# Kernel tuning notes

Measured on AMD Instinct MI355X. Metric: run time of the kernel, lower is better.

The kernel has to match this reference:

```python
import jax, jax.numpy as jnp
import numpy as np

B = 1 << 20
EMB = 8
N_BREEDS, N_TEMPS = 15, 9
HIDDENS = [128, 64, 32]
IN_DIM = (EMB * 2 + 9) * 2  # 50
EPS = 1e-5


def _encode_pet(breed, size, energy, temp, age, social, weight, breed_emb, temp_emb):
    # breed/temp: [B] int -> embedding gather [B,8]; size/energy -> one-hot [B,3]
    be = breed_emb[breed]
    te = temp_emb[temp]
    size_oh = jax.nn.one_hot(size, 3, dtype=be.dtype)
    energy_oh = jax.nn.one_hot(energy, 3, dtype=be.dtype)
    nums = jnp.stack([age / 15.0, social, weight / 100.0], axis=-1)  # [B,3]
    return jnp.concatenate([be, size_oh, energy_oh, te, nums], axis=-1)  # [B,25]


def _mlp(x, Ws, bs, gammas, betas, Wout, bout):
    for W, b, g, bt in zip(Ws, bs, gammas, betas):
        x = x @ W + b
        mu = jnp.mean(x, axis=0)
        var = jnp.mean(jnp.square(x - mu), axis=0)  # biased var (torch BN training)
        x = (x - mu) * jax.lax.rsqrt(var + EPS) * g + bt
        x = jax.nn.relu(x)
    x = x @ Wout + bout
    return jax.nn.sigmoid(x).squeeze(-1)  # [B]


def setup_inputs() -> dict:
    key = jax.random.key(0)
    ks = jax.random.split(key, 32)
    inp = {
        "pet1_breed": jax.random.randint(ks[0], (B,), 0, N_BREEDS, dtype=jnp.int32),
        "pet1_size": jax.random.randint(ks[1], (B,), 0, 3, dtype=jnp.int32),
        "pet1_energy": jax.random.randint(ks[2], (B,), 0, 3, dtype=jnp.int32),
        "pet1_temp": jax.random.randint(ks[3], (B,), 0, N_TEMPS, dtype=jnp.int32),
        "pet1_age": jax.random.uniform(ks[4], (B,)) * 15.0,
        "pet1_social": jax.random.uniform(ks[5], (B,)),
        "pet1_weight": jax.random.uniform(ks[6], (B,)) * 100.0,
        "pet2_breed": jax.random.randint(ks[7], (B,), 0, N_BREEDS, dtype=jnp.int32),
        "pet2_size": jax.random.randint(ks[8], (B,), 0, 3, dtype=jnp.int32),
        "pet2_energy": jax.random.randint(ks[9], (B,), 0, 3, dtype=jnp.int32),
        "pet2_temp": jax.random.randint(ks[10], (B,), 0, N_TEMPS, dtype=jnp.int32),
        "pet2_age": jax.random.uniform(ks[11], (B,)) * 15.0,
        "pet2_social": jax.random.uniform(ks[12], (B,)),
        "pet2_weight": jax.random.uniform(ks[13], (B,)) * 100.0,
        "breed_emb": jax.random.normal(ks[14], (N_BREEDS, EMB), dtype=jnp.float32),
        "temp_emb": jax.random.normal(ks[15], (N_TEMPS, EMB), dtype=jnp.float32),
    }
    prev = IN_DIM
    ki = 16
    for i, h in enumerate(HIDDENS, start=1):
        s = 1.0 / np.sqrt(prev)
        inp[f"W{i}"] = jax.random.uniform(ks[ki], (prev, h), minval=-s, maxval=s); ki += 1
        inp[f"b{i}"] = jax.random.uniform(ks[ki], (h,), minval=-s, maxval=s); ki += 1
        inp[f"gamma{i}"] = jnp.ones((h,), jnp.float32)
        inp[f"beta{i}"] = jnp.zeros((h,), jnp.float32)
        prev = h
    s = 1.0 / np.sqrt(prev)
    inp["W4"] = jax.random.uniform(ks[ki], (prev, 1), minval=-s, maxval=s); ki += 1
    inp["b4"] = jax.random.uniform(ks[ki], (1,), minval=-s, maxval=s)
    return inp


def reference(pet1_breed, pet1_size, pet1_energy, pet1_temp, pet1_age, pet1_social, pet1_weight,
              pet2_breed, pet2_size, pet2_energy, pet2_temp, pet2_age, pet2_social, pet2_weight,
              breed_emb, temp_emb,
              W1, b1, gamma1, beta1, W2, b2, gamma2, beta2, W3, b3, gamma3, beta3, W4, b4):
    f1 = _encode_pet(pet1_breed, pet1_size, pet1_energy, pet1_temp,
                     pet1_age, pet1_social, pet1_weight, breed_emb, temp_emb)
    f2 = _encode_pet(pet2_breed, pet2_size, pet2_energy, pet2_temp,
                     pet2_age, pet2_social, pet2_weight, breed_emb, temp_emb)
    x = jnp.concatenate([f1, f2], axis=-1)  # [B,50]
    return _mlp(x, [W1, W2, W3], [b1, b2, b3], [gamma1, gamma2, gamma3],
                [beta1, beta2, beta3], W4, b4)
```

## Files before the change

kernel.cpp:

```cpp
#include <hip/hip_runtime.h>
#include <hip/hip_bf16.h>

#define BATCH (1u<<20)
static constexpr float EPSBN = 1e-5f;
static constexpr float INV_B = 1.0f / (float)BATCH;

typedef unsigned int   uint;
typedef unsigned short ushort;
typedef unsigned long long u64;

#define TSTR 132
#define NTABROWS 66
#define OFF_W2F    55296ULL
#define OFF_W3F    71680ULL
#define OFF_STATS  75776ULL
#define OFF_PARAMS 90112ULL
#define OFF_W1S    94208ULL
#define OFF_X2     147456ULL
#define OFF_X1     (147456ULL + 134217728ULL)
#define OFF_X3T3   (OFF_X1 + 268435456ULL)
#define T1_NEED    (147456ULL + 134217728ULL)
#define T2_NEED    (OFF_X1 + 67108864ULL)
#define T3_NEED    (OFF_X3T3 + 67108864ULL)

struct Ptrs {
  const int *br1,*sz1,*en1,*tp1; const float *ag1,*so1,*wt1;
  const int *br2,*sz2,*en2,*tp2; const float *ag2,*so2,*wt2;
  const float *bemb,*temb;
  const float *W1,*b1,*g1,*be1;
  const float *W2,*b2,*g2,*be2;
  const float *W3,*b3,*g3,*be3;
  const float *W4,*b4;
  float* ws; float* out;
};

typedef __attribute__((ext_vector_type(8))) short bf16x8;
typedef __attribute__((ext_vector_type(4))) float f32x4;

__device__ __forceinline__ float4 ld4(const float* p) {
  return *reinterpret_cast<const float4*>(p);
}
__device__ __forceinline__ float4 f4add(float4 a, float4 b) {
  return make_float4(a.x+b.x, a.y+b.y, a.z+b.z, a.w+b.w);
}
__device__ __forceinline__ float4 f4fma(float4 a, float4 w, float s) {
  return make_float4(fmaf(w.x,s,a.x), fmaf(w.y,s,a.y), fmaf(w.z,s,a.z), fmaf(w.w,s,a.w));
}
__device__ __forceinline__ void add4(float4& a, const float4 b) {
  a.x += b.x; a.y += b.y; a.z += b.z; a.w += b.w;
}
__device__ __forceinline__ void fma4s(float4& a, const float4 b, float s) {
  a.x = fmaf(b.x, s, a.x); a.y = fmaf(b.y, s, a.y);
  a.z = fmaf(b.z, s, a.z); a.w = fmaf(b.w, s, a.w);
}

__device__ __forceinline__ ushort bfb(float f) {
  union { __hip_bfloat16 h; ushort u; } cv; cv.h = __float2bfloat16(f); return cv.u;
}
__device__ __forceinline__ uint pk2(float a, float b) {
  return ((uint)bfb(b) << 16) | (uint)bfb(a);
}
__device__ __forceinline__ uint pku(ushort a, ushort b) {
  return ((uint)b << 16) | (uint)a;
}
__device__ __forceinline__ bf16x8 ldfrag(const void* p) {
  union { uint4 u; bf16x8 v; } cv; cv.u = *reinterpret_cast<const uint4*>(p); return cv.v;
}
__device__ __forceinline__ bf16x8 mkfrag(uint a, uint b, uint c, uint d) {
  union { uint4 u; bf16x8 v; } cv; cv.u = make_uint4(a,b,c,d); return cv.v;
}
__device__ __forceinline__ float bflo(uint w) { return __uint_as_float(w << 16); }
__device__ __forceinline__ float bfhi(uint w) { return __uint_as_float(w & 0xffff0000u); }
__device__ __forceinline__ float bf2f(ushort u) { return __uint_as_float(((uint)u) << 16); }

struct SIdx { int r[8]; float v[6]; };
__device__ __forceinline__ SIdx load_idx(const Ptrs& P, unsigned s) {
  SIdx o;
  o.r[0] = P.br1[s];      o.r[1] = 15 + P.tp1[s];
  o.r[2] = 24 + P.br2[s]; o.r[3] = 39 + P.tp2[s];
  o.r[4] = 48 + P.sz1[s]; o.r[5] = 51 + P.en1[s];
  o.r[6] = 54 + P.sz2[s]; o.r[7] = 57 + P.en2[s];
  o.v[0] = P.ag1[s]*(1.0f/15.0f); o.v[1] = P.so1[s]; o.v[2] = P.wt1[s]*0.01f;
  o.v[3] = P.ag2[s]*(1.0f/15.0f); o.v[4] = P.so2[s]; o.v[5] = P.wt2[s]*0.01f;
  return o;
}

__device__ __forceinline__ float4 gather4(const float* Tl, const float* contT,
                                          const int rb[8], const float v[6], int c) {
  float4 A = f4add(f4add(ld4(Tl+rb[0]+c), ld4(Tl+rb[1]+c)),
                   f4add(ld4(Tl+rb[2]+c), ld4(Tl+rb[3]+c)));
  float4 B = f4add(f4add(ld4(Tl+rb[4]+c), ld4(Tl+rb[5]+c)),
                   f4add(ld4(Tl+rb[6]+c), ld4(Tl+rb[7]+c)));
  A = f4fma(A, ld4(contT + 60*TSTR + c), v[0]);
  A = f4fma(A, ld4(contT + 61*TSTR + c), v[1]);
  A = f4fma(A, ld4(contT + 62*TSTR + c), v[2]);
  B = f4fma(B, ld4(contT + 63*TSTR + c), v[3]);
  B = f4fma(B, ld4(contT + 64*TSTR + c), v[4]);
  B = f4fma(B, ld4(contT + 65*TSTR + c), v[5]);
  return f4add(A, B);
}

__device__ __forceinline__ void load_rb(const Ptrs& P, unsigned s, int rb[8], float v[6]) {
  SIdx o = load_idx(P, s);
  #pragma unroll
  for (int i = 0; i < 8; ++i) rb[i] = o.r[i]*TSTR;
  #pragma unroll
  for (int i = 0; i < 6; ++i) v[i] = o.v[i];
}

__device__ __forceinline__ void stage_tab(const float* wsT, const float* params,
                                          float* Tl, bool bn1) {
  for (int i = threadIdx.x; i < NTABROWS*TSTR; i += blockDim.x) Tl[i] = wsT[i];
  if (bn1) {
    for (int i = threadIdx.x; i < 128; i += blockDim.x) {
      Tl[66*TSTR + i] = params[i];
      Tl[67*TSTR + i] = params[128 + i];
    }
  }
  __syncthreads();
}

__device__ __forceinline__ void x2_from_lds(const float* Tl, const int rb[8], const float v[6],
                                            const float* W2, const float* b2, float4 acc[16]) {
  #pragma unroll
  for (int j4 = 0; j4 < 16; ++j4) acc[j4] = ld4(b2 + j4*4);
  #pragma unroll 1
  for (int c4 = 0; c4 < 32; ++c4) {
    const int c = c4 * 4;
    float4 x = gather4(Tl, Tl, rb, v, c);
    const float4 sc = *reinterpret_cast<const float4*>(Tl + 66*TSTR + c);
    const float4 sh = *reinterpret_cast<const float4*>(Tl + 67*TSTR + c);
    float hv[4];
    hv[0] = fmaxf(fmaf(x.x, sc.x, sh.x), 0.0f);
    hv[1] = fmaxf(fmaf(x.y, sc.y, sh.y), 0.0f);
    hv[2] = fmaxf(fmaf(x.z, sc.z, sh.z), 0.0f);
    hv[3] = fmaxf(fmaf(x.w, sc.w, sh.w), 0.0f);
    #pragma unroll
    for (int r = 0; r < 4; ++r) {
      const float hr = hv[r];
      const float4* w = reinterpret_cast<const float4*>(W2 + (c + r)*64);
      #pragma unroll
      for (int j4 = 0; j4 < 16; ++j4) fma4s(acc[j4], w[j4], hr);
    }
  }
}

__device__ __forceinline__ void x3_from_acc2(const float4 acc2[16], const Ptrs& P,
                                             const float* sc2, const float* sh2,
                                             float4 acc3[8]) {
  #pragma unroll
  for (int j4 = 0; j4 < 8; ++j4) acc3[j4] = ld4(P.b3 + j4*4);
  #pragma unroll
  for (int k4 = 0; k4 < 16; ++k4) {
    const float4 a = acc2[k4];
    const float4 sc = ld4(sc2 + k4*4), sh = ld4(sh2 + k4*4);
    const float hr[4] = {
      fmaxf(fmaf(a.x, sc.x, sh.x), 0.0f),
      fmaxf(fmaf(a.y, sc.y, sh.y), 0.0f),
      fmaxf(fmaf(a.z, sc.z, sh.z), 0.0f),
      fmaxf(fmaf(a.w, sc.w, sh.w), 0.0f)};
    #pragma unroll
    for (int r = 0; r < 4; ++r) {
      const float4* w = reinterpret_cast<const float4*>(P.W3 + (k4*4 + r)*32);
      #pragma unroll
      for (int j4 = 0; j4 < 8; ++j4) fma4s(acc3[j4], w[j4], hr[r]);
    }
  }
}

__device__ __forceinline__ float bfly_tail32(float st[32], int lane) {
#define BSTEP(D) { const bool h = (lane & D) != 0; \
  _Pragma("unroll") \
  for (int i = 0; i < D; ++i) { \
    float mine = h ? st[i] : st[i+D]; \
    float oth  = __shfl_xor(mine, D, 64); \
    float keep = h ? st[i+D] : st[i]; \
    st[i] = keep + oth; } }
  BSTEP(16) BSTEP(8) BSTEP(4) BSTEP(2) BSTEP(1)
#undef BSTEP
  return st[0];
}

template<bool SQ>
__device__ __forceinline__ float bfly64_from(const float4 acc[16], int lane) {
  float st[32];
  const bool hi = (lane & 32) != 0;
  #pragma unroll
  for (int j4 = 0; j4 < 8; ++j4) {
#define DO1(comp, idx) { \
    float lo = acc[j4].comp, hc = acc[j4+8].comp; \
    if (SQ) { lo *= lo; hc *= hc; } \
    float mine = hi ? lo : hc; \
    float keep = hi ? hc : lo; \
    st[4*j4+idx] = keep + __shfl_xor(mine, 32, 64); }
    DO1(x,0) DO1(y,1) DO1(z,2) DO1(w,3)
#undef DO1
  }
  return bfly_tail32(st, lane);
}

template<bool SQ>
__device__ __forceinline__ float bfly32_from(const float4 acc3[8], int lane) {
  float st[32];
  const bool hi = (lane & 32) != 0;
  #pragma unroll
  for (int j4 = 0; j4 < 8; ++j4) {
#define DO1(comp, idx) { \
    float vv = acc3[j4].comp; \
    if (SQ) vv *= vv; \
    float mine = hi ? vv : 0.0f; \
    float keep = hi ? 0.0f : vv; \
    st[4*j4+idx] = keep + __shfl_xor(mine, 32, 64); }
    DO1(x,0) DO1(y,1) DO1(z,2) DO1(w,3)
#undef DO1
  }
  return bfly_tail32(st, lane);
}

__device__ __forceinline__ int frag_row(int t, int q) {
  if (t < 4)       { if (t == 3 && q == 3) return -1; const int b = 4*t + q; return (b <= 14) ? b : -1; }
  else if (t < 7)  { if (t == 6 && q >= 1) return 60 + (q-1); const int vv = 4*(t-4)+q; return (vv <= 8) ? 15 + vv : -1; }
  else if (t == 7) { return (q <= 2) ? 48 + q : -1; }
  else if (t < 12) { const int b = 4*(t-8)+q; return (b <= 14) ? 24 + b : -1; }
  else if (t < 15) { if (t == 14 && q >= 1) return 63 + (q-1); const int vv = 4*(t-12)+q; return (vv <= 8) ? 39 + vv : -1; }
  else if (t == 15){ return (q <= 2) ? 51 + q : -1; }
  else if (t == 16){ return (q <= 2) ? 54 + q : -1; }
  else if (t == 17){ return (q <= 2) ? 57 + q : -1; }
  return -1;
}


__global__ __launch_bounds__(256) void k_prep(Ptrs P) {
  const int t = threadIdx.x;
  float* T = P.ws;
  {
    float* st = (float*)((char*)P.ws + OFF_STATS);
    for (int i = t; i < 224*16; i += 256) st[i] = 0.0f;
  }
  if (t < 128) {
    const int c = t;
    for (int b = 0; b < 15; ++b) {
      float a1 = P.b1[c], a2 = 0.0f;
      #pragma unroll
      for (int e = 0; e < 8; ++e) {
        a1 = fmaf(P.bemb[b*8+e], P.W1[e*128 + c], a1);
        a2 = fmaf(P.bemb[b*8+e], P.W1[(25+e)*128 + c], a2);
      }
      T[b*TSTR + c] = a1; T[(24+b)*TSTR + c] = a2;
    }
    for (int tt = 0; tt < 9; ++tt) {
      float a1 = 0.0f, a2 = 0.0f;
      #pragma unroll
      for (int e = 0; e < 8; ++e) {
        a1 = fmaf(P.temb[tt*8+e], P.W1[(14+e)*128 + c], a1);
        a2 = fmaf(P.temb[tt*8+e], P.W1[(39+e)*128 + c], a2);
      }
      T[(15+tt)*TSTR + c] = a1; T[(39+tt)*TSTR + c] = a2;
    }
    #pragma unroll
    for (int i = 0; i < 3; ++i) {
      T[(48+i)*TSTR + c] = P.W1[(8+i)*128 + c];
      T[(51+i)*TSTR + c] = P.W1[(11+i)*128 + c];
      T[(54+i)*TSTR + c] = P.W1[(33+i)*128 + c];
      T[(57+i)*TSTR + c] = P.W1[(36+i)*128 + c];
    }
    const int cr[6] = {22,23,24,47,48,49};
    #pragma unroll
    for (int m = 0; m < 6; ++m) T[(60+m)*TSTR + c] = P.W1[cr[m]*128 + c];
  }
  __syncthreads();
  __hip_bfloat16* w2f = (__hip_bfloat16*)((char*)P.ws + OFF_W2F);
  for (int slot = t; slot < 1024; slot += 256) {
    const int fid = slot >> 6, l = slot & 63;
    const int mt = fid >> 2, kk = fid & 3, q = l >> 4, m = l & 15;
    #pragma unroll
    for (int e = 0; e < 8; ++e)
      w2f[slot*8 + e] = __float2bfloat16(P.W2[(kk*32 + 8*q + e)*64 + 16*mt + m]);
  }
  __hip_bfloat16* w3f = (__hip_bfloat16*)((char*)P.ws + OFF_W3F);
  for (int slot = t; slot < 256; slot += 256) {
    const int fid = slot >> 6, l = slot & 63;
    const int mt = fid >> 1, kk = fid & 1, q = l >> 4, m = l & 15;
    #pragma unroll
    for (int e = 0; e < 8; ++e)
      w3f[slot*8 + e] = __float2bfloat16(P.W3[(kk*32 + 8*q + e)*32 + 16*mt + m]);
  }
  uint4* w1s = (uint4*)((char*)P.ws + OFF_W1S);
  for (int slot = t; slot < 3072; slot += 256) {
    const int fid = slot >> 6, l = slot & 63;
    const int hl = fid & 1, mk = fid >> 1;
    const int kk = mk % 3, mt = mk / 3;
    const int q = l >> 4, m = l & 15, ch = 16*mt + m;
    ushort out[8];
    #pragma unroll
    for (int e = 0; e < 8; ++e) {
      const int row = frag_row(8*kk + e, q);
      const float val = (row >= 0) ? T[row*TSTR + ch] : 0.0f;
      const ushort hib = bfb(val);
      out[e] = (hl == 0) ? hib : bfb(val - bf2f(hib));
    }
    w1s[slot] = make_uint4(pku(out[0],out[1]), pku(out[2],out[3]),
                           pku(out[4],out[5]), pku(out[6],out[7]));
  }
}

__global__ __launch_bounds__(512) void k_stats1m(Ptrs P, int storex1) {
  __shared__ __align__(16) char Wl[49152];
  __shared__ float sred[256];
  {
    const uint4* src = (const uint4*)((const char*)P.ws + OFF_W1S);
    uint4* dst = (uint4*)Wl;
    for (int i = threadIdx.x; i < 3072; i += 512) dst[i] = src[i];
  }
  if (threadIdx.x < 256) sred[threadIdx.x] = 0.f;
  __syncthreads();
  const int lane = threadIdx.x & 63;
  const int q = lane >> 4, m16 = lane & 15;
  const unsigned gw = (blockIdx.x*512 + threadIdx.x) >> 6;
  const unsigned nw = (gridDim.x*512) >> 6;
  const int mt0 = (gw & 1) * 4;
  const unsigned ts = nw >> 1;
  const unsigned NT = BATCH >> 4;
  char* x1B = (char*)P.ws + OFF_X1;
  f32x4 sums[4], sqs[4];
  #pragma unroll
  for (int mi = 0; mi < 4; ++mi) { sums[mi] = (f32x4){0,0,0,0}; sqs[mi] = (f32x4){0,0,0,0}; }
  const ushort ONE = 0x3F80;
  for (unsigned it = gw >> 1; it < NT; it += ts) {
    const unsigned s = it*16 + m16;
    const int c0 = P.br1[s], c1 = P.tp1[s], c2 = P.br2[s], c3 = P.tp2[s];
    const int c4i = P.sz1[s], c5 = P.en1[s], c6 = P.sz2[s], c7 = P.en2[s];
    const ushort vb0 = bfb(P.ag1[s]*(1.0f/15.0f)), vb1 = bfb(P.so1[s]);
    const ushort vb2 = bfb(P.wt1[s]*0.01f);
    const ushort vb3 = bfb(P.ag2[s]*(1.0f/15.0f)), vb4 = bfb(P.so2[s]);
    const ushort vb5 = bfb(P.wt2[s]*0.01f);
#define INDE(cv, tgt) ((ushort)(((cv) == (tgt)) ? ONE : 0))
    const ushort e0 = INDE(c0, q),     e1 = INDE(c0, 4+q);
    const ushort e2 = INDE(c0, 8+q);
    const ushort e3 = (q == 3) ? ONE : INDE(c0, 12+q);
    const ushort e4 = INDE(c1, q),     e5 = INDE(c1, 4+q);
    const ushort e6 = (q == 0) ? INDE(c1, 8)
                               : ((q == 1) ? vb0 : (q == 2) ? vb1 : vb2);
    const ushort e7 = INDE(c4i, q);
    const ushort f0 = INDE(c2, q),     f1 = INDE(c2, 4+q);
    const ushort f2 = INDE(c2, 8+q),   f3 = INDE(c2, 12+q);
    const ushort f4 = INDE(c3, q),     f5 = INDE(c3, 4+q);
    const ushort f6 = (q == 0) ? INDE(c3, 8)
                               : ((q == 1) ? vb3 : (q == 2) ? vb4 : vb5);
    const ushort f7 = INDE(c5, q);
    const ushort g0 = INDE(c6, q),     g1 = INDE(c7, q);
#undef INDE
    const bf16x8 B0 = mkfrag(pku(e0,e1), pku(e2,e3), pku(e4,e5), pku(e6,e7));
    const bf16x8 B1 = mkfrag(pku(f0,f1), pku(f2,f3), pku(f4,f5), pku(f6,f7));
    const bf16x8 B2 = mkfrag(pku(g0,g1), 0u, 0u, 0u);
    #pragma unroll
    for (int mi = 0; mi < 4; ++mi) {
      const int mt = mt0 + mi;
      f32x4 D = (f32x4){0.f,0.f,0.f,0.f};
      #pragma unroll
      for (int kk = 0; kk < 3; ++kk) {
        const bf16x8 bf = (kk == 0) ? B0 : (kk == 1) ? B1 : B2;
        const bf16x8 ah = ldfrag(Wl + (size_t)(((mt*3+kk)*2+0)*64 + lane)*16);
        D = __builtin_amdgcn_mfma_f32_16x16x32_bf16(ah, bf, D, 0, 0, 0);
        const bf16x8 al = ldfrag(Wl + (size_t)(((mt*3+kk)*2+1)*64 + lane)*16);
        D = __builtin_amdgcn_mfma_f32_16x16x32_bf16(al, bf, D, 0, 0, 0);
      }
      if (storex1) {
        const uint lo = pk2(D[0], D[1]);
        const uint hi = pk2(D[2], D[3]);
        *reinterpret_cast<uint2*>(x1B + (size_t)s*256 + (16*mt + 4*q)*2) = make_uint2(lo, hi);
      }
      #pragma unroll
      for (int r = 0; r < 4; ++r) {
        sums[mi][r] += D[r];
        sqs[mi][r]   = fmaf(D[r], D[r], sqs[mi][r]);
      }
    }
  }
  #pragma unroll
  for (int d = 1; d <= 8; d <<= 1) {
    #pragma unroll
    for (int mi = 0; mi < 4; ++mi) {
      #pragma unroll
      for (int r = 0; r < 4; ++r) {
        sums[mi][r] += __shfl_xor(sums[mi][r], d, 64);
        sqs[mi][r]  += __shfl_xor(sqs[mi][r],  d, 64);
      }
    }
  }
  if (m16 == 0) {
    #pragma unroll
    for (int mi = 0; mi < 4; ++mi) {
      #pragma unroll
      for (int r = 0; r < 4; ++r) {
        const int ch = 16*(mt0 + mi) + 4*q + r;
        atomicAdd(&sred[ch], sums[mi][r]);
        atomicAdd(&sred[128+ch], sqs[mi][r]);
      }
    }
  }
  __syncthreads();
  if (threadIdx.x < 128) {
    float* stat = (float*)((char*)P.ws + OFF_STATS) + (size_t)threadIdx.x*16;
    atomicAdd(stat,     sred[threadIdx.x]);
    atomicAdd(stat + 8, sred[128+threadIdx.x]);
  }
}

__global__ __launch_bounds__(256) void k_l2x(Ptrs P) {
  __shared__ __align__(16) float bn[256];
  if (threadIdx.x < 128) {
    const float* stat = (const float*)((const char*)P.ws + OFF_STATS) + (size_t)threadIdx.x*16;
    const float mean = stat[0] * INV_B;
    const float var  = stat[8] * INV_B - mean*mean;
    const float scale = P.g1[threadIdx.x] / sqrtf(var + EPSBN);
    bn[threadIdx.x]       = scale;
    bn[128 + threadIdx.x] = P.be1[threadIdx.x] - mean * scale;
  }
  __syncthreads();
  const int lane = threadIdx.x & 63;
  const int q = lane >> 4, m16 = lane & 15;
  const char* w2fB = (const char*)P.ws + OFF_W2F;
  const char* x1B = (const char*)P.ws + OFF_X1;
  char* x2B = (char*)P.ws + OFF_X2;
  const unsigned nw = (gridDim.x*256) >> 6;
  const unsigned NT = BATCH >> 4;
  unsigned it = (blockIdx.x*256 + threadIdx.x) >> 6;
  if (it >= NT) return;
  unsigned s = it*16 + m16;
  uint4 x0 = *reinterpret_cast<const uint4*>(x1B + (size_t)s*256 +   0 + q*16);
  uint4 x1 = *reinterpret_cast<const uint4*>(x1B + (size_t)s*256 +  64 + q*16);
  uint4 x2 = *reinterpret_cast<const uint4*>(x1B + (size_t)s*256 + 128 + q*16);
  uint4 x3 = *reinterpret_cast<const uint4*>(x1B + (size_t)s*256 + 192 + q*16);
  while (true) {
    const unsigned itn = it + nw;
    const bool more = itn < NT;
    uint4 n0, n1, n2, n3;
    if (more) {
      const size_t rb = (size_t)(itn*16 + m16)*256;
      n0 = *reinterpret_cast<const uint4*>(x1B + rb +   0 + q*16);
      n1 = *reinterpret_cast<const uint4*>(x1B + rb +  64 + q*16);
      n2 = *reinterpret_cast<const uint4*>(x1B + rb + 128 + q*16);
      n3 = *reinterpret_cast<const uint4*>(x1B + rb + 192 + q*16);
    }
    f32x4 D[4];
    #pragma unroll
    for (int mt = 0; mt < 4; ++mt) {
      const float4 b = ld4(P.b2 + 16*mt + 4*q);
      D[mt][0] = b.x; D[mt][1] = b.y; D[mt][2] = b.z; D[mt][3] = b.w;
    }
    #pragma unroll
    for (int kk = 0; kk < 4; ++kk) {
      const uint4 u = (kk == 0) ? x0 : (kk == 1) ? x1 : (kk == 2) ? x2 : x3;
      const int c = kk*32 + 8*q;
      const float4 scA = ld4(bn + c), shA = ld4(bn + 128 + c);
      const float4 scB = ld4(bn + c + 4), shB = ld4(bn + 128 + c + 4);
      const uint w[4] = {u.x,u.y,u.z,u.w};
      const float h0 = fmaxf(fmaf(bflo(w[0]), scA.x, shA.x), 0.f);
      const float h1 = fmaxf(fmaf(bfhi(w[0]), scA.y, shA.y), 0.f);
      const float h2 = fmaxf(fmaf(bflo(w[1]), scA.z, shA.z), 0.f);
      const float h3 = fmaxf(fmaf(bfhi(w[1]), scA.w, shA.w), 0.f);
      const float h4 = fmaxf(fmaf(bflo(w[2]), scB.x, shB.x), 0.f);
      const float h5 = fmaxf(fmaf(bfhi(w[2]), scB.y, shB.y), 0.f);
      const float h6 = fmaxf(fmaf(bflo(w[3]), scB.z, shB.z), 0.f);
      const float h7 = fmaxf(fmaf(bfhi(w[3]), scB.w, shB.w), 0.f);
      const bf16x8 bf = mkfrag(pk2(h0,h1), pk2(h2,h3), pk2(h4,h5), pk2(h6,h7));
      #pragma unroll
      for (int mt = 0; mt < 4; ++mt) {
        const bf16x8 af = ldfrag(w2fB + (size_t)((mt*4+kk)*64 + lane)*16);
        D[mt] = __builtin_amdgcn_mfma_f32_16x16x32_bf16(af, bf, D[mt], 0, 0, 0);
      }
    }
    #pragma unroll
    for (int mt = 0; mt < 4; ++mt) {
      const uint lo = pk2(D[mt][0], D[mt][1]);
      const uint hi = pk2(D[mt][2], D[mt][3]);
      *reinterpret_cast<uint2*>(x2B + (size_t)s*128 + (16*mt + 4*q)*2) = make_uint2(lo, hi);
    }
    if (!more) break;
    x0 = n0; x1 = n1; x2 = n2; x3 = n3; it = itn; s = it*16 + m16;
  }
}

__global__ __launch_bounds__(512) void k_l2m(Ptrs P) {
  __shared__ __align__(16) float Tl[60*TSTR];
  __shared__ __align__(16) float bn[256];
  for (int i = threadIdx.x; i < 60*TSTR; i += 512) Tl[i] = P.ws[i];
  if (threadIdx.x < 128) {
    const float* stat = (const float*)((const char*)P.ws + OFF_STATS) + (size_t)threadIdx.x*16;
    const float mean = stat[0] * INV_B;
    const float var  = stat[8] * INV_B - mean*mean;
    const float scale = P.g1[threadIdx.x] / sqrtf(var + EPSBN);
    bn[threadIdx.x]       = scale;
    bn[128 + threadIdx.x] = P.be1[threadIdx.x] - mean * scale;
  }
  __syncthreads();
  const float* contT = P.ws;
  const int lane = threadIdx.x & 63;
  const int q = lane >> 4, m16 = lane & 15;
  const char* w2fB = (const char*)P.ws + OFF_W2F;
  char* x2B = (char*)P.ws + OFF_X2;
  const unsigned nw = (gridDim.x*512) >> 6;
  const unsigned NT = BATCH >> 4;
  unsigned it = (blockIdx.x*512 + threadIdx.x) >> 6;
  if (it >= NT) return;
  SIdx cur = load_idx(P, it*16 + m16);
  while (true) {
    const unsigned itn = it + nw;
    const bool more = itn < NT;
    SIdx nxt;
    if (more) nxt = load_idx(P, itn*16 + m16);
    const unsigned s = it*16 + m16;
    int rb[8];
    #pragma unroll
    for (int i = 0; i < 8; ++i) rb[i] = cur.r[i]*TSTR;
    f32x4 D[4];
    #pragma unroll
    for (int mt = 0; mt < 4; ++mt) {
      const float4 b = ld4(P.b2 + 16*mt + 4*q);
      D[mt][0] = b.x; D[mt][1] = b.y; D[mt][2] = b.z; D[mt][3] = b.w;
    }
    #pragma unroll
    for (int kk = 0; kk < 4; ++kk) {
      const int c = kk*32 + 8*q;
      const float4 xa = gather4(Tl, contT, rb, cur.v, c);
      const float4 xb = gather4(Tl, contT, rb, cur.v, c + 4);
      const float4 sca = ld4(bn + c), sha = ld4(bn + 128 + c);
      const float4 scb = ld4(bn + c + 4), shb = ld4(bn + 128 + c + 4);
      const float h0 = fmaxf(fmaf(xa.x, sca.x, sha.x), 0.f);
      const float h1 = fmaxf(fmaf(xa.y, sca.y, sha.y), 0.f);
      const float h2 = fmaxf(fmaf(xa.z, sca.z, sha.z), 0.f);
      const float h3 = fmaxf(fmaf(xa.w, sca.w, sha.w), 0.f);
      const float h4 = fmaxf(fmaf(xb.x, scb.x, shb.x), 0.f);
      const float h5 = fmaxf(fmaf(xb.y, scb.y, shb.y), 0.f);
      const float h6 = fmaxf(fmaf(xb.z, scb.z, shb.z), 0.f);
      const float h7 = fmaxf(fmaf(xb.w, scb.w, shb.w), 0.f);
      const bf16x8 bf = mkfrag(pk2(h0,h1), pk2(h2,h3), pk2(h4,h5), pk2(h6,h7));
      #pragma unroll
      for (int mt = 0; mt < 4; ++mt) {
        const bf16x8 af = ldfrag(w2fB + (size_t)((mt*4+kk)*64 + lane)*16);
        D[mt] = __builtin_amdgcn_mfma_f32_16x16x32_bf16(af, bf, D[mt], 0, 0, 0);
      }
    }
    #pragma unroll
    for (int mt = 0; mt < 4; ++mt) {
      const uint lo = pk2(D[mt][0], D[mt][1]);
      const uint hi = pk2(D[mt][2], D[mt][3]);
      *reinterpret_cast<uint2*>(x2B + (size_t)s*128 + (16*mt + 4*q)*2) = make_uint2(lo, hi);
    }
    if (!more) break;
    cur = nxt; it = itn;
  }
}

__global__ __launch_bounds__(512) void k_stats1(Ptrs P) {
  __shared__ __align__(16) float Tl[60*TSTR];
  __shared__ float sred[256];
  for (int i = threadIdx.x; i < 60*TSTR; i += 512) Tl[i] = P.ws[i];
  if (threadIdx.x < 256) sred[threadIdx.x] = 0.f;
  __syncthreads();
  const int lane = threadIdx.x & 63;
  const int q = lane >> 4, m16 = lane & 15;
  const float* contT = P.ws;
  const unsigned gw = (blockIdx.x*512 + threadIdx.x) >> 6;
  const unsigned nw = (gridDim.x*512) >> 6;
  const int kk = gw & 3;
  const int c = kk*32 + 8*q;
  const unsigned NT = BATCH >> 4;
  unsigned it = gw >> 2;
  const unsigned ts = nw >> 2;
  float4 sa = make_float4(0,0,0,0), sb = sa, qa = sa, qb = sa;
  bool active = it < NT;
  int rb[8]; float v[6];
  if (active) load_rb(P, it*16 + m16, rb, v);
  while (active) {
    const unsigned itn = it + ts;
    const bool more = itn < NT;
    int rbn[8]; float vn[6];
    if (more) load_rb(P, itn*16 + m16, rbn, vn);
    const float4 xa = gather4(Tl, contT, rb, v, c);
    const float4 xb = gather4(Tl, contT, rb, v, c + 4);
    add4(sa, xa); add4(sb, xb);
    qa.x = fmaf(xa.x, xa.x, qa.x); qa.y = fmaf(xa.y, xa.y, qa.y);
    qa.z = fmaf(xa.z, xa.z, qa.z); qa.w = fmaf(xa.w, xa.w, qa.w);
    qb.x = fmaf(xb.x, xb.x, qb.x); qb.y = fmaf(xb.y, xb.y, qb.y);
    qb.z = fmaf(xb.z, xb.z, qb.z); qb.w = fmaf(xb.w, xb.w, qb.w);
    if (!more) break;
    #pragma unroll
    for (int i = 0; i < 8; ++i) rb[i] = rbn[i];
    #pragma unroll
    for (int i = 0; i < 6; ++i) v[i] = vn[i];
    it = itn;
  }
  #pragma unroll
  for (int d = 1; d <= 8; d <<= 1) {
    sa.x += __shfl_xor(sa.x, d, 64); sa.y += __shfl_xor(sa.y, d, 64);
    sa.z += __shfl_xor(sa.z, d, 64); sa.w += __shfl_xor(sa.w, d, 64);
    sb.x += __shfl_xor(sb.x, d, 64); sb.y += __shfl_xor(sb.y, d, 64);
    sb.z += __shfl_xor(sb.z, d, 64); sb.w += __shfl_xor(sb.w, d, 64);
    qa.x += __shfl_xor(qa.x, d, 64); qa.y += __shfl_xor(qa.y, d, 64);
    qa.z += __shfl_xor(qa.z, d, 64); qa.w += __shfl_xor(qa.w, d, 64);
    qb.x += __shfl_xor(qb.x, d, 64); qb.y += __shfl_xor(qb.y, d, 64);
    qb.z += __shfl_xor(qb.z, d, 64); qb.w += __shfl_xor(qb.w, d, 64);
  }
  if (m16 == 0) {
    atomicAdd(&sred[c+0], sa.x); atomicAdd(&sred[c+1], sa.y);
    atomicAdd(&sred[c+2], sa.z); atomicAdd(&sred[c+3], sa.w);
    atomicAdd(&sred[c+4], sb.x); atomicAdd(&sred[c+5], sb.y);
    atomicAdd(&sred[c+6], sb.z); atomicAdd(&sred[c+7], sb.w);
    atomicAdd(&sred[128+c+0], qa.x); atomicAdd(&sred[128+c+1], qa.y);
    atomicAdd(&sred[128+c+2], qa.z); atomicAdd(&sred[128+c+3], qa.w);
    atomicAdd(&sred[128+c+4], qb.x); atomicAdd(&sred[128+c+5], qb.y);
    atomicAdd(&sred[128+c+6], qb.z); atomicAdd(&sred[128+c+7], qb.w);
  }
  __syncthreads();
  if (threadIdx.x < 128) {
    float* stat = (float*)((char*)P.ws + OFF_STATS) + (size_t)threadIdx.x*16;
    atomicAdd(stat,     sred[threadIdx.x]);
    atomicAdd(stat + 8, sred[128+threadIdx.x]);
  }
}

__global__ void k_finalize(Ptrs P, int nch, int entry0, int pofs,
                           const float* g, const float* be) {
  const int c = threadIdx.x;
  if (c >= nch) return;
  const float* stat = (const float*)((const char*)P.ws + OFF_STATS) + (size_t)(entry0 + c)*16;
  const float mean = stat[0] * INV_B;
  const float var  = stat[8] * INV_B - mean*mean;
  const float inv  = 1.0f / sqrtf(var + EPSBN);
  const float scale = g[c] * inv;
  float* params = (float*)((char*)P.ws + OFF_PARAMS);
  params[pofs + c]       = scale;
  params[pofs + nch + c] = be[c] - mean * scale;
}

__global__ __launch_bounds__(256) void k_stats2(Ptrs P) {
  const uint* x2u = (const uint*)((const char*)P.ws + OFF_X2);
  const int pid = threadIdx.x & 31;
  const int lane = threadIdx.x & 63;
  const int w = threadIdx.x >> 6;
  float slo = 0.f, shi = 0.f, qlo = 0.f, qhi = 0.f;
  const unsigned r0 = blockIdx.x*8 + (threadIdx.x >> 5);
  const unsigned rs = gridDim.x*8;
  #pragma unroll 4
  for (unsigned r = r0; r < BATCH; r += rs) {
    const uint u = x2u[(size_t)r*32 + pid];
    const float lo = bflo(u), hi = bfhi(u);
    slo += lo; shi += hi;
    qlo = fmaf(lo, lo, qlo); qhi = fmaf(hi, hi, qhi);
  }
  slo += __shfl_xor(slo, 32, 64); shi += __shfl_xor(shi, 32, 64);
  qlo += __shfl_xor(qlo, 32, 64); qhi += __shfl_xor(qhi, 32, 64);
  __shared__ float red[512];
  if (lane < 32) {
    red[w*64 + 2*pid]       = slo; red[w*64 + 2*pid + 1]       = shi;
    red[256 + w*64 + 2*pid] = qlo; red[256 + w*64 + 2*pid + 1] = qhi;
  }
  __syncthreads();
  if (threadIdx.x < 64) {
    const int c = threadIdx.x;
    const float s  = red[c] + red[64+c] + red[128+c] + red[192+c];
    const float qq = red[256+c] + red[320+c] + red[384+c] + red[448+c];
    float* stat = (float*)((char*)P.ws + OFF_STATS) + (size_t)(128 + c)*16;
    atomicAdd(stat, s); atomicAdd(stat + 8, qq);
  }
}

__global__ __launch_bounds__(256) void k_l3m(Ptrs P, u64 x3off, int x3str) {
  __shared__ __align__(16) float bn[128];
  if (threadIdx.x < 64) {
    const float* stat = (const float*)((const char*)P.ws + OFF_STATS) + (size_t)(128 + threadIdx.x)*16;
    const float mean = stat[0] * INV_B;
    const float var  = stat[8] * INV_B - mean*mean;
    const float scale = P.g2[threadIdx.x] / sqrtf(var + EPSBN);
    bn[threadIdx.x]      = scale;
    bn[64 + threadIdx.x] = P.be2[threadIdx.x] - mean * scale;
  }
  __syncthreads();
  const int lane = threadIdx.x & 63;
  const int q = lane >> 4, m16 = lane & 15;
  const char* w3fB = (const char*)P.ws + OFF_W3F;
  const char* xB = (const char*)P.ws + OFF_X2;
  char* x3B = (char*)P.ws + x3off;
  const unsigned nw = (gridDim.x*256) >> 6;
  const unsigned NT = BATCH >> 4;
  unsigned it = (blockIdx.x*256 + threadIdx.x) >> 6;
  if (it >= NT) return;
  unsigned s = it*16 + m16;
  uint4 u0 = *reinterpret_cast<const uint4*>(xB + (size_t)s*128 + q*16);
  uint4 u1 = *reinterpret_cast<const uint4*>(xB + (size_t)s*128 + 64 + q*16);
  while (true) {
    const unsigned itn = it + nw;
    const bool more = itn < NT;
    uint4 n0, n1;
    if (more) {
      const unsigned sn = itn*16 + m16;
      n0 = *reinterpret_cast<const uint4*>(xB + (size_t)sn*128 + q*16);
      n1 = *reinterpret_cast<const uint4*>(xB + (size_t)sn*128 + 64 + q*16);
    }
    f32x4 D[2];
    #pragma unroll
    for (int mt = 0; mt < 2; ++mt) {
      const float4 b = ld4(P.b3 + 16*mt + 4*q);
// ... 86 lines not shown
    #pragma unroll
    for (int c16 = 0; c16 < 4; ++c16) {
      const uint4 u = *reinterpret_cast<const uint4*>(xB + (size_t)s*x3str + c16*16);
      const uint w[4] = {u.x,u.y,u.z,u.w};
      #pragma unroll
      for (int j = 0; j < 4; ++j) {
        const int ch = c16*8 + 2*j;
        const float hlo = fmaxf(fmaf(bflo(w[j]), sc3[ch],   sh3[ch]),   0.f);
        const float hhi = fmaxf(fmaf(bfhi(w[j]), sc3[ch+1], sh3[ch+1]), 0.f);
        z = fmaf(hlo, P.W4[ch], z);
        z = fmaf(hhi, P.W4[ch+1], z);
      }
    }
    P.out[s] = 1.0f / (1.0f + __expf(-z));
  }
}

__global__ __launch_bounds__(256) void k_l2r(Ptrs P) {
  __shared__ __align__(16) float Tl[68*TSTR];
  __shared__ float red[512];
  const float* params = (const float*)((const char*)P.ws + OFF_PARAMS);
  stage_tab(P.ws, params, Tl, true);
  const int lane = threadIdx.x & 63;
  float4 sums[16], sqs[16];
  #pragma unroll
  for (int j4 = 0; j4 < 16; ++j4) {
    sums[j4] = make_float4(0.f,0.f,0.f,0.f);
    sqs[j4]  = make_float4(0.f,0.f,0.f,0.f);
  }
  const unsigned stride = gridDim.x * 256;
  for (unsigned s = blockIdx.x*256 + threadIdx.x; s < BATCH; s += stride) {
    int rb[8]; float v[6];
    load_rb(P, s, rb, v);
    float4 acc[16];
    x2_from_lds(Tl, rb, v, P.W2, P.b2, acc);
    #pragma unroll
    for (int j4 = 0; j4 < 16; ++j4) {
      add4(sums[j4], acc[j4]);
      sqs[j4].x = fmaf(acc[j4].x, acc[j4].x, sqs[j4].x);
      sqs[j4].y = fmaf(acc[j4].y, acc[j4].y, sqs[j4].y);
      sqs[j4].z = fmaf(acc[j4].z, acc[j4].z, sqs[j4].z);
      sqs[j4].w = fmaf(acc[j4].w, acc[j4].w, sqs[j4].w);
    }
  }
  const float psum = bfly64_from<false>(sums, lane);
  const float psq  = bfly64_from<false>(sqs,  lane);
  red[threadIdx.x] = psum; red[256 + threadIdx.x] = psq;
  __syncthreads();
  const int t = threadIdx.x;
  if (t < 64) {
    const float s0 = red[t] + red[t+64] + red[t+128] + red[t+192];
    const float q0 = red[256+t] + red[256+t+64] + red[256+t+128] + red[256+t+192];
    float* stat = (float*)((char*)P.ws + OFF_STATS) + (size_t)(128 + t)*16;
    atomicAdd(stat, s0); atomicAdd(stat + 8, q0);
  }
}

__global__ __launch_bounds__(256) void k_l3_rec(Ptrs P) {
  __shared__ __align__(16) float Tl[68*TSTR];
  __shared__ float red[512];
  const float* params = (const float*)((const char*)P.ws + OFF_PARAMS);
  stage_tab(P.ws, params, Tl, true);
  const float* sc2 = params + 256, *sh2 = params + 320;
  const int lane = threadIdx.x & 63;
  float4 sums3[8], sqs3[8];
  #pragma unroll
  for (int j4 = 0; j4 < 8; ++j4) {
    sums3[j4] = make_float4(0.f,0.f,0.f,0.f);
    sqs3[j4]  = make_float4(0.f,0.f,0.f,0.f);
  }
  const unsigned stride = gridDim.x * 256;
  for (unsigned s = blockIdx.x*256 + threadIdx.x; s < BATCH; s += stride) {
    int rb[8]; float v[6];
    load_rb(P, s, rb, v);
    float4 acc2[16];
    x2_from_lds(Tl, rb, v, P.W2, P.b2, acc2);
    float4 acc3[8];
    x3_from_acc2(acc2, P, sc2, sh2, acc3);
    #pragma unroll
    for (int j4 = 0; j4 < 8; ++j4) {
      add4(sums3[j4], acc3[j4]);
      sqs3[j4].x = fmaf(acc3[j4].x, acc3[j4].x, sqs3[j4].x);
      sqs3[j4].y = fmaf(acc3[j4].y, acc3[j4].y, sqs3[j4].y);
      sqs3[j4].z = fmaf(acc3[j4].z, acc3[j4].z, sqs3[j4].z);
      sqs3[j4].w = fmaf(acc3[j4].w, acc3[j4].w, sqs3[j4].w);
    }
  }
  const float psum = bfly32_from<false>(sums3, lane);
  const float psq  = bfly32_from<false>(sqs3,  lane);
  red[threadIdx.x] = psum; red[256 + threadIdx.x] = psq;
  __syncthreads();
  const int t = threadIdx.x;
  if (t < 32) {
    const float s0 = red[t] + red[t+64] + red[t+128] + red[t+192];
    const float q0 = red[256+t] + red[256+t+64] + red[256+t+128] + red[256+t+192];
    float* stat = (float*)((char*)P.ws + OFF_STATS) + (size_t)(192 + t)*16;
    atomicAdd(stat, s0); atomicAdd(stat + 8, q0);
  }
}

__global__ __launch_bounds__(256) void k_l4_rec(Ptrs P) {
  __shared__ __align__(16) float Tl[68*TSTR];
  const float* params = (const float*)((const char*)P.ws + OFF_PARAMS);
  stage_tab(P.ws, params, Tl, true);
  const float* sc2 = params + 256, *sh2 = params + 320;
  const float* sc3 = params + 384, *sh3 = params + 416;
  const unsigned stride = gridDim.x * 256;
  for (unsigned s = blockIdx.x*256 + threadIdx.x; s < BATCH; s += stride) {
    int rb[8]; float v[6];
    load_rb(P, s, rb, v);
    float4 acc2[16];
    x2_from_lds(Tl, rb, v, P.W2, P.b2, acc2);
    float4 acc3[8];
    x3_from_acc2(acc2, P, sc2, sh2, acc3);
    float z = P.b4[0];
    #pragma unroll
    for (int k4 = 0; k4 < 8; ++k4) {
      const float4 a = acc3[k4];
      const float4 sc = ld4(sc3 + k4*4), sh = ld4(sh3 + k4*4);
      z = fmaf(fmaxf(fmaf(a.x, sc.x, sh.x), 0.0f), P.W4[k4*4+0], z);
      z = fmaf(fmaxf(fmaf(a.y, sc.y, sh.y), 0.0f), P.W4[k4*4+1], z);
      z = fmaf(fmaxf(fmaf(a.z, sc.z, sh.z), 0.0f), P.W4[k4*4+2], z);
      z = fmaf(fmaxf(fmaf(a.w, sc.w, sh.w), 0.0f), P.W4[k4*4+3], z);
    }
    P.out[s] = 1.0f / (1.0f + __expf(-z));
  }
}


extern "C" void kernel_launch(void* const* d_in, const int* in_sizes, int n_in,
                              void* d_out, int out_size, void* d_ws, size_t ws_size,
                              hipStream_t stream) {
  Ptrs P;
  P.br1 = (const int*)d_in[0];  P.sz1 = (const int*)d_in[1];
  P.en1 = (const int*)d_in[2];  P.tp1 = (const int*)d_in[3];
  P.ag1 = (const float*)d_in[4]; P.so1 = (const float*)d_in[5]; P.wt1 = (const float*)d_in[6];
  P.br2 = (const int*)d_in[7];  P.sz2 = (const int*)d_in[8];
  P.en2 = (const int*)d_in[9];  P.tp2 = (const int*)d_in[10];
  P.ag2 = (const float*)d_in[11]; P.so2 = (const float*)d_in[12]; P.wt2 = (const float*)d_in[13];
  P.bemb = (const float*)d_in[14]; P.temb = (const float*)d_in[15];
  P.W1 = (const float*)d_in[16]; P.b1 = (const float*)d_in[17];
  P.g1 = (const float*)d_in[18]; P.be1 = (const float*)d_in[19];
  P.W2 = (const float*)d_in[20]; P.b2 = (const float*)d_in[21];
  P.g2 = (const float*)d_in[22]; P.be2 = (const float*)d_in[23];
  P.W3 = (const float*)d_in[24]; P.b3 = (const float*)d_in[25];
  P.g3 = (const float*)d_in[26]; P.be3 = (const float*)d_in[27];
  P.W4 = (const float*)d_in[28]; P.b4 = (const float*)d_in[29];
  P.ws = (float*)d_ws; P.out = (float*)d_out;

  const bool t1 = ws_size >= T1_NEED;
  const bool t2 = ws_size >= T2_NEED;
  const bool t3 = ws_size >= T3_NEED;
  u64 x3off; int x3str;
  if (t3)      { x3off = OFF_X3T3; x3str = 64; }
  else if (t2) { x3off = OFF_X1;   x3str = 64; }
  else         { x3off = OFF_X2;   x3str = 128; }

  hipLaunchKernelGGL(k_prep, dim3(1), dim3(256), 0, stream, P);
  if (t3) {
    hipLaunchKernelGGL(k_stats1m, dim3(1024), dim3(512), 0, stream, P, 1);
    hipLaunchKernelGGL(k_l2x, dim3(2048), dim3(256), 0, stream, P);
    hipLaunchKernelGGL(k_stats2, dim3(1024), dim3(256), 0, stream, P);
    hipLaunchKernelGGL(k_l3m, dim3(2048), dim3(256), 0, stream, P, x3off, x3str);
    hipLaunchKernelGGL(k_stats3, dim3(1024), dim3(256), 0, stream, P, x3off, x3str/4);
    hipLaunchKernelGGL(k_l4n, dim3(2048), dim3(256), 0, stream, P, x3off, x3str);
  } else if (t1) {
    hipLaunchKernelGGL(k_stats1m, dim3(1024), dim3(512), 0, stream, P, 0);
    hipLaunchKernelGGL(k_l2m, dim3(1024), dim3(512), 0, stream, P);
    hipLaunchKernelGGL(k_stats2, dim3(1024), dim3(256), 0, stream, P);
    hipLaunchKernelGGL(k_l3m, dim3(2048), dim3(256), 0, stream, P, x3off, x3str);
    hipLaunchKernelGGL(k_stats3, dim3(1024), dim3(256), 0, stream, P, x3off, x3str/4);
    hipLaunchKernelGGL(k_l4n, dim3(2048), dim3(256), 0, stream, P, x3off, x3str);
  } else {
    hipLaunchKernelGGL(k_stats1, dim3(1024), dim3(512), 0, stream, P);
    hipLaunchKernelGGL(k_finalize, dim3(1), dim3(128), 0, stream, P, 128, 0, 0, P.g1, P.be1);
    hipLaunchKernelGGL(k_l2r, dim3(1024), dim3(256), 0, stream, P);
    hipLaunchKernelGGL(k_finalize, dim3(1), dim3(64), 0, stream, P, 64, 128, 256, P.g2, P.be2);
    hipLaunchKernelGGL(k_l3_rec, dim3(1024), dim3(256), 0, stream, P);
    hipLaunchKernelGGL(k_finalize, dim3(1), dim3(32), 0, stream, P, 32, 192, 384, P.g3, P.be3);
    hipLaunchKernelGGL(k_l4_rec, dim3(2048), dim3(256), 0, stream, P);
  }
}
```

Before: 557.9 us.

## Recompute layer-1 with MFMA inside layer-2 kernel and store x3 in place over x2

Replaces the table-gather layer-2 kernel on the t1 path with k_l2f. It rebuilds the one-hot/numeric bf16 fragments from the raw inputs, recomputes layer 1 with MFMA, applies BN1 and ReLU, then shuffles the results into layer-2 MFMA operands without staging x1. On the t3 path, x3 now overwrites the x2 buffer, which lowers the workspace needed to enable that path. This trades scalar LDS gather work for extra MFMA and shuffle work, and relies on each thread reading its x2 row before writing x3 to the same location.

Result: slower. 809.0 us (+45.0%).

```diff
diff --git a/kernel.cpp b/kernel.cpp
--- a/kernel.cpp
+++ b/kernel.cpp
@@ -18,10 +18,9 @@
 #define OFF_W1S    94208ULL
 #define OFF_X2     147456ULL
 #define OFF_X1     (147456ULL + 134217728ULL)
-#define OFF_X3T3   (OFF_X1 + 268435456ULL)
 #define T1_NEED    (147456ULL + 134217728ULL)
 #define T2_NEED    (OFF_X1 + 67108864ULL)
-#define T3_NEED    (OFF_X3T3 + 67108864ULL)
+#define T3_NEED    (OFF_X1 + 268435456ULL)
 
 struct Ptrs {
   const int *br1,*sz1,*en1,*tp1; const float *ag1,*so1,*wt1;
@@ -83,6 +82,42 @@
   o.v[0] = P.ag1[s]*(1.0f/15.0f); o.v[1] = P.so1[s]; o.v[2] = P.wt1[s]*0.01f;
   o.v[3] = P.ag2[s]*(1.0f/15.0f); o.v[4] = P.so2[s]; o.v[5] = P.wt2[s]*0.01f;
   return o;
+}
+
+struct Raw { int c[8]; float v[6]; };
+__device__ __forceinline__ Raw load_raw(const Ptrs& P, unsigned s) {
+  Raw o;
+  o.c[0] = P.br1[s]; o.c[1] = P.tp1[s]; o.c[2] = P.br2[s]; o.c[3] = P.tp2[s];
+  o.c[4] = P.sz1[s]; o.c[5] = P.en1[s]; o.c[6] = P.sz2[s]; o.c[7] = P.en2[s];
+  o.v[0] = P.ag1[s]*(1.0f/15.0f); o.v[1] = P.so1[s]; o.v[2] = P.wt1[s]*0.01f;
+  o.v[3] = P.ag2[s]*(1.0f/15.0f); o.v[4] = P.so2[s]; o.v[5] = P.wt2[s]*0.01f;
+  return o;
+}
+
+__device__ __forceinline__ void build_bfrags(const Raw& o, int q,
+                                             bf16x8& B0, bf16x8& B1, bf16x8& B2) {
+  const ushort ONE = 0x3F80;
+  const ushort vb0 = bfb(o.v[0]), vb1 = bfb(o.v[1]), vb2 = bfb(o.v[2]);
+  const ushort vb3 = bfb(o.v[3]), vb4 = bfb(o.v[4]), vb5 = bfb(o.v[5]);
+#define INDE(cv, tgt) ((ushort)(((cv) == (tgt)) ? ONE : 0))
+  const ushort e0 = INDE(o.c[0], q),     e1 = INDE(o.c[0], 4+q);
+  const ushort e2 = INDE(o.c[0], 8+q);
+  const ushort e3 = (q == 3) ? ONE : INDE(o.c[0], 12+q);
+  const ushort e4 = INDE(o.c[1], q),     e5 = INDE(o.c[1], 4+q);
+  const ushort e6 = (q == 0) ? INDE(o.c[1], 8)
+                             : ((q == 1) ? vb0 : (q == 2) ? vb1 : vb2);
+  const ushort e7 = INDE(o.c[4], q);
+  const ushort f0 = INDE(o.c[2], q),     f1 = INDE(o.c[2], 4+q);
+  const ushort f2 = INDE(o.c[2], 8+q),   f3 = INDE(o.c[2], 12+q);
+  const ushort f4 = INDE(o.c[3], q),     f5 = INDE(o.c[3], 4+q);
+  const ushort f6 = (q == 0) ? INDE(o.c[3], 8)
+                             : ((q == 1) ? vb3 : (q == 2) ? vb4 : vb5);
+  const ushort f7 = INDE(o.c[5], q);
+  const ushort g0 = INDE(o.c[6], q),     g1 = INDE(o.c[7], q);
+#undef INDE
+  B0 = mkfrag(pku(e0,e1), pku(e2,e3), pku(e4,e5), pku(e6,e7));
+  B1 = mkfrag(pku(f0,f1), pku(f2,f3), pku(f4,f5), pku(f6,f7));
+  B2 = mkfrag(pku(g0,g1), 0u, 0u, 0u);
 }
 
 __device__ __forceinline__ float4 gather4(const float* Tl, const float* contT,
@@ -325,34 +360,11 @@
   f32x4 sums[4], sqs[4];
   #pragma unroll
   for (int mi = 0; mi < 4; ++mi) { sums[mi] = (f32x4){0,0,0,0}; sqs[mi] = (f32x4){0,0,0,0}; }
-  const ushort ONE = 0x3F80;
   for (unsigned it = gw >> 1; it < NT; it += ts) {
     const unsigned s = it*16 + m16;
-    const int c0 = P.br1[s], c1 = P.tp1[s], c2 = P.br2[s], c3 = P.tp2[s];
-    const int c4i = P.sz1[s], c5 = P.en1[s], c6 = P.sz2[s], c7 = P.en2[s];
-    const ushort vb0 = bfb(P.ag1[s]*(1.0f/15.0f)), vb1 = bfb(P.so1[s]);
-    const ushort vb2 = bfb(P.wt1[s]*0.01f);
-    const ushort vb3 = bfb(P.ag2[s]*(1.0f/15.0f)), vb4 = bfb(P.so2[s]);
-    const ushort vb5 = bfb(P.wt2[s]*0.01f);
-#define INDE(cv, tgt) ((ushort)(((cv) == (tgt)) ? ONE : 0))
-    const ushort e0 = INDE(c0, q),     e1 = INDE(c0, 4+q);
-    const ushort e2 = INDE(c0, 8+q);
-    const ushort e3 = (q == 3) ? ONE : INDE(c0, 12+q);
-    const ushort e4 = INDE(c1, q),     e5 = INDE(c1, 4+q);
-    const ushort e6 = (q == 0) ? INDE(c1, 8)
-                               : ((q == 1) ? vb0 : (q == 2) ? vb1 : vb2);
-    const ushort e7 = INDE(c4i, q);
-    const ushort f0 = INDE(c2, q),     f1 = INDE(c2, 4+q);
-    const ushort f2 = INDE(c2, 8+q),   f3 = INDE(c2, 12+q);
-    const ushort f4 = INDE(c3, q),     f5 = INDE(c3, 4+q);
-    const ushort f6 = (q == 0) ? INDE(c3, 8)
-                               : ((q == 1) ? vb3 : (q == 2) ? vb4 : vb5);
-    const ushort f7 = INDE(c5, q);
-    const ushort g0 = INDE(c6, q),     g1 = INDE(c7, q);
-#undef INDE
-    const bf16x8 B0 = mkfrag(pku(e0,e1), pku(e2,e3), pku(e4,e5), pku(e6,e7));
-    const bf16x8 B1 = mkfrag(pku(f0,f1), pku(f2,f3), pku(f4,f5), pku(f6,f7));
-    const bf16x8 B2 = mkfrag(pku(g0,g1), 0u, 0u, 0u);
+    const Raw o = load_raw(P, s);
+    bf16x8 B0, B1, B2;
+    build_bfrags(o, q, B0, B1, B2);
     #pragma unroll
     for (int mi = 0; mi < 4; ++mi) {
       const int mt = mt0 + mi;
@@ -404,6 +416,96 @@
     float* stat = (float*)((char*)P.ws + OFF_STATS) + (size_t)threadIdx.x*16;
     atomicAdd(stat,     sred[threadIdx.x]);
     atomicAdd(stat + 8, sred[128+threadIdx.x]);
+  }
+}
+
+__global__ __launch_bounds__(512) void k_l2f(Ptrs P) {
+  __shared__ __align__(16) char Wl[49152];
+  __shared__ __align__(16) float bn[256];
+  {
+    const uint4* src = (const uint4*)((const char*)P.ws + OFF_W1S);
+    uint4* dst = (uint4*)Wl;
+    for (int i = threadIdx.x; i < 3072; i += 512) dst[i] = src[i];
+  }
+  if (threadIdx.x < 128) {
+    const float* stat = (const float*)((const char*)P.ws + OFF_STATS) + (size_t)threadIdx.x*16;
+    const float mean = stat[0] * INV_B;
+    const float var  = stat[8] * INV_B - mean*mean;
+    const float scale = P.g1[threadIdx.x] / sqrtf(var + EPSBN);
+    bn[threadIdx.x]       = scale;
+    bn[128 + threadIdx.x] = P.be1[threadIdx.x] - mean * scale;
+  }
+  __syncthreads();
+  const int lane = threadIdx.x & 63;
+  const int q = lane >> 4, m16 = lane & 15;
+  const char* w2fB = (const char*)P.ws + OFF_W2F;
+  char* x2B = (char*)P.ws + OFF_X2;
+  const unsigned nw = (gridDim.x*512) >> 6;
+  const unsigned NT = BATCH >> 4;
+  unsigned it = (blockIdx.x*512 + threadIdx.x) >> 6;
+  if (it >= NT) return;
+  Raw cur = load_raw(P, it*16 + m16);
+  while (true) {
+    const unsigned itn = it + nw;
+    const bool more = itn < NT;
+    Raw nxt;
+    if (more) nxt = load_raw(P, itn*16 + m16);
+    const unsigned s = it*16 + m16;
+    bf16x8 B0, B1, B2;
+    build_bfrags(cur, q, B0, B1, B2);
+    uint pkh[8][2];
+    #pragma unroll
+    for (int mt = 0; mt < 8; ++mt) {
+      f32x4 D = (f32x4){0.f,0.f,0.f,0.f};
+      #pragma unroll
+      for (int kk = 0; kk < 3; ++kk) {
+        const bf16x8 bf = (kk == 0) ? B0 : (kk == 1) ? B1 : B2;
+        const bf16x8 ah = ldfrag(Wl + (size_t)(((mt*3+kk)*2+0)*64 + lane)*16);
+        D = __builtin_amdgcn_mfma_f32_16x16x32_bf16(ah, bf, D, 0, 0, 0);
+        const bf16x8 al = ldfrag(Wl + (size_t)(((mt*3+kk)*2+1)*64 + lane)*16);
+        D = __builtin_amdgcn_mfma_f32_16x16x32_bf16(al, bf, D, 0, 0, 0);
+      }
+      const int c = 16*mt + 4*q;
+      const float4 sc4 = *reinterpret_cast<const float4*>(bn + c);
+      const float4 sh4 = *reinterpret_cast<const float4*>(bn + 128 + c);
+      const float h0 = fmaxf(fmaf(D[0], sc4.x, sh4.x), 0.f);
+      const float h1 = fmaxf(fmaf(D[1], sc4.y, sh4.y), 0.f);
+      const float h2 = fmaxf(fmaf(D[2], sc4.z, sh4.z), 0.f);
+      const float h3 = fmaxf(fmaf(D[3], sc4.w, sh4.w), 0.f);
+      pkh[mt][0] = pk2(h0, h1);
+      pkh[mt][1] = pk2(h2, h3);
+    }
+    f32x4 D2[4];
+    #pragma unroll
+    for (int mt2 = 0; mt2 < 4; ++mt2) {
+      const float4 b = ld4(P.b2 + 16*mt2 + 4*q);
+      D2[mt2][0] = b.x; D2[mt2][1] = b.y; D2[mt2][2] = b.z; D2[mt2][3] = b.w;
+    }
+    #pragma unroll
+    for (int kk2 = 0; kk2 < 4; ++kk2) {
+      uint fw[4];
+      #pragma unroll
+      for (int w2 = 0; w2 < 4; ++w2) {
+        const int src = ((2*(q & 1) + (w2 >> 1)) << 4) | m16;
+        const uint ua = (uint)__shfl((int)pkh[2*kk2][w2 & 1], src, 64);
+        const uint ub = (uint)__shfl((int)pkh[2*kk2+1][w2 & 1], src, 64);
+        fw[w2] = (q & 2) ? ub : ua;
+      }
+      const bf16x8 bf2 = mkfrag(fw[0], fw[1], fw[2], fw[3]);
+      #pragma unroll
+      for (int mt2 = 0; mt2 < 4; ++mt2) {
+        const bf16x8 af = ldfrag(w2fB + (size_t)((mt2*4+kk2)*64 + lane)*16);
+        D2[mt2] = __builtin_amdgcn_mfma_f32_16x16x32_bf16(af, bf2, D2[mt2], 0, 0, 0);
+      }
+    }
+    #pragma unroll
+    for (int mt2 = 0; mt2 < 4; ++mt2) {
+      const uint lo = pk2(D2[mt2][0], D2[mt2][1]);
+      const uint hi = pk2(D2[mt2][2], D2[mt2][3]);
+      *reinterpret_cast<uint2*>(x2B + (size_t)s*128 + (16*mt2 + 4*q)*2) = make_uint2(lo, hi);
+    }
+    if (!more) break;
+    cur = nxt; it = itn;
   }
 }
 
@@ -479,77 +581,6 @@
     }
     if (!more) break;
     x0 = n0; x1 = n1; x2 = n2; x3 = n3; it = itn; s = it*16 + m16;
-  }
-}
-
-__global__ __launch_bounds__(512) void k_l2m(Ptrs P) {
-  __shared__ __align__(16) float Tl[60*TSTR];
-  __shared__ __align__(16) float bn[256];
-  for (int i = threadIdx.x; i < 60*TSTR; i += 512) Tl[i] = P.ws[i];
-  if (threadIdx.x < 128) {
-    const float* stat = (const float*)((const char*)P.ws + OFF_STATS) + (size_t)threadIdx.x*16;
-    const float mean = stat[0] * INV_B;
-    const float var  = stat[8] * INV_B - mean*mean;
-    const float scale = P.g1[threadIdx.x] / sqrtf(var + EPSBN);
-    bn[threadIdx.x]       = scale;
-    bn[128 + threadIdx.x] = P.be1[threadIdx.x] - mean * scale;
-  }
-  __syncthreads();
-  const float* contT = P.ws;
-  const int lane = threadIdx.x & 63;
-  const int q = lane >> 4, m16 = lane & 15;
-  const char* w2fB = (const char*)P.ws + OFF_W2F;
-  char* x2B = (char*)P.ws + OFF_X2;
-  const unsigned nw = (gridDim.x*512) >> 6;
-  const unsigned NT = BATCH >> 4;
-  unsigned it = (blockIdx.x*512 + threadIdx.x) >> 6;
-  if (it >= NT) return;
-  SIdx cur = load_idx(P, it*16 + m16);
-  while (true) {
-    const unsigned itn = it + nw;
-    const bool more = itn < NT;
-    SIdx nxt;
-    if (more) nxt = load_idx(P, itn*16 + m16);
-    const unsigned s = it*16 + m16;
-    int rb[8];
-    #pragma unroll
-    for (int i = 0; i < 8; ++i) rb[i] = cur.r[i]*TSTR;
-    f32x4 D[4];
-    #pragma unroll
-    for (int mt = 0; mt < 4; ++mt) {
-      const float4 b = ld4(P.b2 + 16*mt + 4*q);
-      D[mt][0] = b.x; D[mt][1] = b.y; D[mt][2] = b.z; D[mt][3] = b.w;
-    }
-    #pragma unroll
-    for (int kk = 0; kk < 4; ++kk) {
-      const int c = kk*32 + 8*q;
-      const float4 xa = gather4(Tl, contT, rb, cur.v, c);
-      const float4 xb = gather4(Tl, contT, rb, cur.v, c + 4);
-      const float4 sca = ld4(bn + c), sha = ld4(bn + 128 + c);
-      const float4 scb = ld4(bn + c + 4), shb = ld4(bn + 128 + c + 4);
-      const float h0 = fmaxf(fmaf(xa.x, sca.x, sha.x), 0.f);
-      const float h1 = fmaxf(fmaf(xa.y, sca.y, sha.y), 0.f);
-      const float h2 = fmaxf(fmaf(xa.z, sca.z, sha.z), 0.f);
-      const float h3 = fmaxf(fmaf(xa.w, sca.w, sha.w), 0.f);
-      const float h4 = fmaxf(fmaf(xb.x, scb.x, shb.x), 0.f);
-      const float h5 = fmaxf(fmaf(xb.y, scb.y, shb.y), 0.f);
-      const float h6 = fmaxf(fmaf(xb.z, scb.z, shb.z), 0.f);
-      const float h7 = fmaxf(fmaf(xb.w, scb.w, shb.w), 0.f);
-      const bf16x8 bf = mkfrag(pk2(h0,h1), pk2(h2,h3), pk2(h4,h5), pk2(h6,h7));
-      #pragma unroll
-      for (int mt = 0; mt < 4; ++mt) {
-        const bf16x8 af = ldfrag(w2fB + (size_t)((mt*4+kk)*64 + lane)*16);
-        D[mt] = __builtin_amdgcn_mfma_f32_16x16x32_bf16(af, bf, D[mt], 0, 0, 0);
-      }
-    }
-    #pragma unroll
-    for (int mt = 0; mt < 4; ++mt) {
-      const uint lo = pk2(D[mt][0], D[mt][1]);
-      const uint hi = pk2(D[mt][2], D[mt][3]);
-      *reinterpret_cast<uint2*>(x2B + (size_t)s*128 + (16*mt + 4*q)*2) = make_uint2(lo, hi);
-    }
-    if (!more) break;
-    cur = nxt; it = itn;
   }
 }
 
@@ -942,9 +973,9 @@
   const bool t2 = ws_size >= T2_NEED;
   const bool t3 = ws_size >= T3_NEED;
   u64 x3off; int x3str;
-  if (t3)      { x3off = OFF_X3T3; x3str = 64; }
-  else if (t2) { x3off = OFF_X1;   x3str = 64; }
-  else         { x3off = OFF_X2;   x3str = 128; }
+  if (t3)      { x3off = OFF_X2; x3str = 128; }
+  else if (t2) { x3off = OFF_X1; x3str = 64; }
+  else         { x3off = OFF_X2; x3str = 128; }
 
   hipLaunchKernelGGL(k_prep, dim3(1), dim3(256), 0, stream, P);
   if (t3) {
@@ -956,7 +987,7 @@
     hipLaunchKernelGGL(k_l4n, dim3(2048), dim3(256), 0, stream, P, x3off, x3str);
   } else if (t1) {
     hipLaunchKernelGGL(k_stats1m, dim3(1024), dim3(512), 0, stream, P, 0);
-    hipLaunchKernelGGL(k_l2m, dim3(1024), dim3(512), 0, stream, P);
+    hipLaunchKernelGGL(k_l2f, dim3(1024), dim3(512), 0, stream, P);
     hipLaunchKernelGGL(k_stats2, dim3(1024), dim3(256), 0, stream, P);
     hipLaunchKernelGGL(k_l3m, dim3(2048), dim3(256), 0, stream, P, x3off, x3str);
     hipLaunchKernelGGL(k_stats3, dim3(1024), dim3(256), 0, stream, P, x3off, x3str/4);
```
